# Performance work log

Measured on AMD Instinct MI355X. Metric: run time of the kernel, lower is better.

Reference implementation:

```python
import jax, jax.numpy as jnp
import numpy as np

D_MODEL = 1024
EXPANDED = 1024  # d_model * expansion_factor(1.0)
K = 3
EPS = 1e-8


def rms_norm(x, w, eps=EPS):
    return x * jax.lax.rsqrt(jnp.mean(x * x, axis=-1, keepdims=True) + eps) * w


def setup_inputs() -> dict:
    key = jax.random.key(0)
    ks = jax.random.split(key, 8)
    b, t = 4, 4096
    u = jax.random.normal(ks[0], (b, t, D_MODEL), dtype=jnp.float32)
    s_in = 1.0 / np.sqrt(D_MODEL)
    s_out = 1.0 / np.sqrt(EXPANDED)
    W_in = jax.random.uniform(ks[1], (2 * EXPANDED, D_MODEL), jnp.float32, -s_in, s_in)
    b_in = jax.random.uniform(ks[2], (2 * EXPANDED,), jnp.float32, -s_in, s_in)
    in_norm_w = jnp.ones((2 * EXPANDED,), jnp.float32)
    s_conv = 1.0 / np.sqrt(K)  # groups=expanded_dim -> fan_in = K
    conv_w = jax.random.uniform(ks[3], (EXPANDED, 1, K), jnp.float32, -s_conv, s_conv)
    conv_b = jax.random.uniform(ks[4], (EXPANDED,), jnp.float32, -s_conv, s_conv)
    W_out = jax.random.uniform(ks[5], (D_MODEL, EXPANDED), jnp.float32, -s_out, s_out)
    b_out = jax.random.uniform(ks[6], (D_MODEL,), jnp.float32, -s_out, s_out)
    out_norm_w = jnp.ones((D_MODEL,), jnp.float32)
    return {
        "u": u, "W_in": W_in, "b_in": b_in, "in_norm_w": in_norm_w,
        "conv_w": conv_w, "conv_b": conv_b,
        "W_out": W_out, "b_out": b_out, "out_norm_w": out_norm_w,
    }


def reference(u, W_in, b_in, in_norm_w, conv_w, conv_b, W_out, b_out, out_norm_w):
    # in_proj + RMSNorm
    xv = rms_norm(jnp.einsum('btd,ed->bte', u, W_in) + b_in, in_norm_w)  # [b,t,2E]
    x, v = jnp.split(xv, 2, axis=-1)  # each [b,t,E]
    # depthwise 'same' conv along time: NCH layout
    x_f = jnp.transpose(x, (0, 2, 1))  # [b,E,t]
    pad = (K - 1) // 2
    y = jax.lax.conv_general_dilated(
        x_f, conv_w, window_strides=(1,), padding=[(pad, pad)],
        dimension_numbers=('NCH', 'OIH', 'NCH'), feature_group_count=EXPANDED)
    y = y + conv_b[None, :, None]
    x_mixed = jnp.transpose(y, (0, 2, 1))  # [b,t,E]
    gated = v * x_mixed
    out = rms_norm(jnp.einsum('bte,de->btd', gated, W_out) + b_out, out_norm_w)
    return out
```

## Files before the change

### kernel.cpp

```cpp
#include <hip/hip_runtime.h>

#define BT    16384
#define TSEQ  4096
#define DM    1024
#define EXP   1024
#define N1    2048
#define KDIM  1024
#define EPSV  1e-8f

typedef __bf16 bf16x8 __attribute__((ext_vector_type(8)));
typedef float f32x16 __attribute__((ext_vector_type(16)));
typedef unsigned short u16x8 __attribute__((ext_vector_type(8)));

#define AS1CAST(p) ((__attribute__((address_space(1))) void*)(p))
#define AS3CAST(p) ((__attribute__((address_space(3))) void*)(p))

__device__ __forceinline__ unsigned short f2bf(float f) {
    unsigned int u = __float_as_uint(f);
    u += 0x7fffu + ((u >> 16) & 1u);
    return (unsigned short)(u >> 16);
}

__global__ __launch_bounds__(256) void k_f2bf(const float* __restrict__ in,
                                              unsigned short* __restrict__ out,
                                              int n4) {
    int i = blockIdx.x * 256 + threadIdx.x;
    if (i >= n4) return;
    float4 v = ((const float4*)in)[i];
    ushort4 o;
    o.x = f2bf(v.x); o.y = f2bf(v.y); o.z = f2bf(v.z); o.w = f2bf(v.w);
    ((ushort4*)out)[i] = o;
}

template <int BF16_OUT>
__device__ __forceinline__ void gemm_body(const unsigned short* __restrict__ A,
                                          const unsigned short* __restrict__ Bw,
                                          const float* __restrict__ bias,
                                          unsigned short* __restrict__ Cb,
                                          float* __restrict__ Cf,
                                          float* __restrict__ ssq,
                                          int N) {
    __shared__ unsigned short sA[128 * 32];
    __shared__ unsigned short sB[128 * 32];

    const int tid  = threadIdx.x;
    const int lane = tid & 63;
    const int wv   = tid >> 6;
    const int wm   = wv >> 1, wn = wv & 1;
    const int row0 = blockIdx.y * 128, col0 = blockIdx.x * 128;

    const int rA = tid >> 2, cA = (tid & 3) * 8;
    const unsigned short* aP = A  + (size_t)(row0 + rA) * KDIM + cA;
    const unsigned short* bP = Bw + (size_t)(col0 + rA) * KDIM + cA;
    unsigned short* lA0 = sA + (wv * 64) * 8;
    unsigned short* lA1 = sA + (256 + wv * 64) * 8;
    unsigned short* lB0 = sB + (wv * 64) * 8;
    unsigned short* lB1 = sB + (256 + wv * 64) * 8;

    const int ln = lane & 31;
    const int hi = lane >> 5;
    const int abase = (wm * 64 + ln) * 32 + hi * 8;
    const int bbase = (wn * 64 + ln) * 32 + hi * 8;

    f32x16 acc[2][2] = {};

    for (int kt = 0; kt < KDIM / 32; ++kt) {
        __syncthreads();
        const unsigned short* ap = aP + kt * 32;
        const unsigned short* bp = bP + kt * 32;
        __builtin_amdgcn_global_load_lds(AS1CAST(ap), AS3CAST(lA0), 16, 0, 0);
        __builtin_amdgcn_global_load_lds(AS1CAST(ap + (size_t)64 * KDIM), AS3CAST(lA1), 16, 0, 0);
        __builtin_amdgcn_global_load_lds(AS1CAST(bp), AS3CAST(lB0), 16, 0, 0);
        __builtin_amdgcn_global_load_lds(AS1CAST(bp + (size_t)64 * KDIM), AS3CAST(lB1), 16, 0, 0);
        __syncthreads();

        bf16x8 aF[2][2], bF[2][2];
#pragma unroll
        for (int i = 0; i < 2; ++i)
#pragma unroll
            for (int ks = 0; ks < 2; ++ks) {
                aF[i][ks] = *(const bf16x8*)&sA[abase + i * 32 * 32 + ks * 16];
                bF[i][ks] = *(const bf16x8*)&sB[bbase + i * 32 * 32 + ks * 16];
            }
#pragma unroll
        for (int ks = 0; ks < 2; ++ks)
#pragma unroll
            for (int i = 0; i < 2; ++i)
#pragma unroll
                for (int j = 0; j < 2; ++j)
                    acc[i][j] = __builtin_amdgcn_mfma_f32_32x32x16_bf16(
                        aF[i][ks], bF[j][ks], acc[i][j], 0, 0, 0);
    }

    const int c0 = col0 + wn * 64 + ln;
    const float bs0 = bias[c0], bs1 = bias[c0 + 32];

#pragma unroll
    for (int i = 0; i < 2; ++i) {
        const int rbase = row0 + wm * 64 + i * 32 + 4 * hi;
#pragma unroll
        for (int reg = 0; reg < 16; ++reg) {
            const int gm = rbase + (reg & 3) + 8 * (reg >> 2);
            float v0 = acc[i][0][reg] + bs0;
            float v1 = acc[i][1][reg] + bs1;
            float p = v0 * v0 + v1 * v1;
#pragma unroll
            for (int off = 1; off < 32; off <<= 1) p += __shfl_xor(p, off, 64);
            if (ln == 0) atomicAdd(&ssq[gm], p);
            size_t base = (size_t)gm * N + c0;
            if (BF16_OUT) {
                Cb[base]      = f2bf(v0);
                Cb[base + 32] = f2bf(v1);
            } else {
                Cf[base]      = v0;
                Cf[base + 32] = v1;
            }
        }
    }
}

__global__ __launch_bounds__(256) void k_gemm_in(const unsigned short* __restrict__ A,
                                                 const unsigned short* __restrict__ Bw,
                                                 const float* __restrict__ bias,
                                                 unsigned short* __restrict__ Cb,
                                                 float* __restrict__ ssq) {
    gemm_body<1>(A, Bw, bias, Cb, nullptr, ssq, N1);
}

__global__ __launch_bounds__(256) void k_gemm_out(const unsigned short* __restrict__ A,
                                                  const unsigned short* __restrict__ Bw,
                                                  const float* __restrict__ bias,
                                                  float* __restrict__ Cf,
                                                  float* __restrict__ ssq) {
    gemm_body<0>(A, Bw, bias, nullptr, Cf, ssq, DM);
}

__global__ __launch_bounds__(256) void k_conv_gate(const unsigned short* __restrict__ z,
                                                   const float* __restrict__ ssq1,
                                                   const float* __restrict__ inw,
                                                   const float* __restrict__ cw,
                                                   const float* __restrict__ cb,
                                                   unsigned short* __restrict__ g) {
    const int tok = blockIdx.x * 2 + (threadIdx.x >> 7);
    const int e8  = (threadIdx.x & 127) * 8;
    const int t   = tok & (TSEQ - 1);

    const float rs0 = rsqrtf(ssq1[tok] * (1.0f / N1) + EPSV);
    const int tm = (t > 0) ? tok - 1 : tok;
    const int tp = (t < TSEQ - 1) ? tok + 1 : tok;
    const float rsm = (t > 0) ? rsqrtf(ssq1[tm] * (1.0f / N1) + EPSV) : 0.0f;
    const float rsp = (t < TSEQ - 1) ? rsqrtf(ssq1[tp] * (1.0f / N1) + EPSV) : 0.0f;

    bf16x8 xm = *(const bf16x8*)(z + (size_t)tm * N1 + e8);
    bf16x8 x0 = *(const bf16x8*)(z + (size_t)tok * N1 + e8);
    bf16x8 xp = *(const bf16x8*)(z + (size_t)tp * N1 + e8);
    bf16x8 vv = *(const bf16x8*)(z + (size_t)tok * N1 + EXP + e8);

    u16x8 ov;
#pragma unroll
    for (int p = 0; p < 8; ++p) {
        const int e = e8 + p;
        const float we  = inw[e];
        const float wvv = inw[EXP + e];
        const float w0 = cw[e * 3], w1 = cw[e * 3 + 1], w2 = cw[e * 3 + 2];
        float y = w0 * ((float)xm[p] * rsm * we)
                + w1 * ((float)x0[p] * rs0 * we)
                + w2 * ((float)xp[p] * rsp * we)
                + cb[e];
        float vn = (float)vv[p] * rs0 * wvv;
        ov[p] = f2bf(vn * y);
    }
    *(u16x8*)(g + (size_t)tok * EXP + e8) = ov;
}

__global__ __launch_bounds__(256) void k_outnorm(float* __restrict__ o,
                                                 const float* __restrict__ ssq2,
                                                 const float* __restrict__ onw) {
    const int idx = blockIdx.x * 256 + threadIdx.x;
    const int tok = idx >> 8;
    const int d4  = (idx & 255) * 4;
    const float rs = rsqrtf(ssq2[tok] * (1.0f / DM) + EPSV);
    float4 v = ((float4*)o)[idx];
    float4 w = *(const float4*)(onw + d4);
    v.x *= rs * w.x; v.y *= rs * w.y; v.z *= rs * w.z; v.w *= rs * w.w;
    ((float4*)o)[idx] = v;
}

extern "C" void kernel_launch(void* const* d_in, const int* in_sizes, int n_in,
                              void* d_out, int out_size, void* d_ws, size_t ws_size,
                              hipStream_t stream) {
    const float* u     = (const float*)d_in[0];
    const float* W_in  = (const float*)d_in[1];
    const float* b_in  = (const float*)d_in[2];
    const float* inw   = (const float*)d_in[3];
    const float* cw    = (const float*)d_in[4];
    const float* cb    = (const float*)d_in[5];
    const float* W_out = (const float*)d_in[6];
    const float* b_out = (const float*)d_in[7];
    const float* onw   = (const float*)d_in[8];
    float* out = (float*)d_out;

    char* ws = (char*)d_ws;
    unsigned short* u_bf    = (unsigned short*)ws; ws += (size_t)BT * DM * 2;
    unsigned short* Win_bf  = (unsigned short*)ws; ws += (size_t)N1 * DM * 2;
    unsigned short* Wout_bf = (unsigned short*)ws; ws += (size_t)DM * EXP * 2;
    unsigned short* z_bf    = (unsigned short*)ws; ws += (size_t)BT * N1 * 2;
    unsigned short* g_bf    = (unsigned short*)ws; ws += (size_t)BT * EXP * 2;
    float* ssq1 = (float*)ws; ws += (size_t)BT * 4;
    float* ssq2 = (float*)ws; ws += (size_t)BT * 4;

    hipMemsetAsync(ssq1, 0, (size_t)BT * 2 * sizeof(float), stream);

    k_f2bf<<<(BT * DM / 4 + 255) / 256, 256, 0, stream>>>(u, u_bf, BT * DM / 4);
    k_f2bf<<<(N1 * DM / 4 + 255) / 256, 256, 0, stream>>>(W_in, Win_bf, N1 * DM / 4);
    k_f2bf<<<(DM * EXP / 4 + 255) / 256, 256, 0, stream>>>(W_out, Wout_bf, DM * EXP / 4);

    dim3 gA(N1 / 128, BT / 128);
    k_gemm_in<<<gA, 256, 0, stream>>>(u_bf, Win_bf, b_in, z_bf, ssq1);

    k_conv_gate<<<BT / 2, 256, 0, stream>>>(z_bf, ssq1, inw, cw, cb, g_bf);

    dim3 gC(DM / 128, BT / 128);
    k_gemm_out<<<gC, 256, 0, stream>>>(g_bf, Wout_bf, b_out, out, ssq2);

    k_outnorm<<<BT, 256, 0, stream>>>(out, ssq2, onw);

    (void)in_sizes; (void)n_in; (void)out_size; (void)ws_size;
}
```

Before: 350.4 us.

## Double GEMM K-tile to 64 with XOR-swizzled LDS layout and merge conversion launches

The GEMM K-step grows from 32 to 64, which halves the number of barrier pairs per tile. The LDS layout gets a row-dependent XOR-style swizzle of the 16-byte chunks so that the MFMA fragment reads avoid bank conflicts. The three fp32-to-bf16 conversion kernels are also merged into one launch. LDS use doubles to 32KB per block, which may lower occupancy, and there is still no double buffering.

```diff
diff --git a/kernel.cpp b/kernel.cpp
--- a/kernel.cpp
+++ b/kernel.cpp
@@ -21,11 +21,15 @@
     return (unsigned short)(u >> 16);
 }
 
-__global__ __launch_bounds__(256) void k_f2bf(const float* __restrict__ in,
-                                              unsigned short* __restrict__ out,
-                                              int n4) {
+__global__ __launch_bounds__(256) void k_f2bf3(const float* __restrict__ i0, unsigned short* __restrict__ o0, int n0,
+                                               const float* __restrict__ i1, unsigned short* __restrict__ o1, int n1,
+                                               const float* __restrict__ i2, unsigned short* __restrict__ o2, int n2) {
     int i = blockIdx.x * 256 + threadIdx.x;
-    if (i >= n4) return;
+    const float* in; unsigned short* out;
+    if (i < n0)                { in = i0; out = o0; }
+    else if (i < n0 + n1)      { in = i1; out = o1; i -= n0; }
+    else if (i < n0 + n1 + n2) { in = i2; out = o2; i -= n0 + n1; }
+    else return;
     float4 v = ((const float4*)in)[i];
     ushort4 o;
     o.x = f2bf(v.x); o.y = f2bf(v.y); o.z = f2bf(v.z); o.w = f2bf(v.w);
@@ -40,8 +44,8 @@
                                           float* __restrict__ Cf,
                                           float* __restrict__ ssq,
                                           int N) {
-    __shared__ unsigned short sA[128 * 32];
-    __shared__ unsigned short sB[128 * 32];
+    __shared__ unsigned short sA[128 * 64];
+    __shared__ unsigned short sB[128 * 64];
 
     const int tid  = threadIdx.x;
     const int lane = tid & 63;
@@ -49,47 +53,56 @@
     const int wm   = wv >> 1, wn = wv & 1;
     const int row0 = blockIdx.y * 128, col0 = blockIdx.x * 128;
 
-    const int rA = tid >> 2, cA = (tid & 3) * 8;
-    const unsigned short* aP = A  + (size_t)(row0 + rA) * KDIM + cA;
-    const unsigned short* bP = Bw + (size_t)(col0 + rA) * KDIM + cA;
-    unsigned short* lA0 = sA + (wv * 64) * 8;
-    unsigned short* lA1 = sA + (256 + wv * 64) * 8;
-    unsigned short* lB0 = sB + (wv * 64) * 8;
-    unsigned short* lB1 = sB + (256 + wv * 64) * 8;
+    const int p7 = tid & 7;
+    const unsigned short* aPtr[4];
+    const unsigned short* bPtr[4];
+#pragma unroll
+    for (int b = 0; b < 4; ++b) {
+        const int r = (b * 256 + tid) >> 3;
+        const int q = (p7 - r) & 7;
+        aPtr[b] = A  + (size_t)(row0 + r) * KDIM + q * 8;
+        bPtr[b] = Bw + (size_t)(col0 + r) * KDIM + q * 8;
+    }
+    unsigned short* lA[4];
+    unsigned short* lB[4];
+#pragma unroll
+    for (int b = 0; b < 4; ++b) {
+        lA[b] = sA + (b * 256 + wv * 64) * 8;
+        lB[b] = sB + (b * 256 + wv * 64) * 8;
+    }
 
     const int ln = lane & 31;
     const int hi = lane >> 5;
-    const int abase = (wm * 64 + ln) * 32 + hi * 8;
-    const int bbase = (wn * 64 + ln) * 32 + hi * 8;
+    const int arow0 = (wm * 64 + ln) * 64;
+    const int brow0 = (wn * 64 + ln) * 64;
 
     f32x16 acc[2][2] = {};
 
-    for (int kt = 0; kt < KDIM / 32; ++kt) {
+    for (int kt = 0; kt < KDIM / 64; ++kt) {
         __syncthreads();
-        const unsigned short* ap = aP + kt * 32;
-        const unsigned short* bp = bP + kt * 32;
-        __builtin_amdgcn_global_load_lds(AS1CAST(ap), AS3CAST(lA0), 16, 0, 0);
-        __builtin_amdgcn_global_load_lds(AS1CAST(ap + (size_t)64 * KDIM), AS3CAST(lA1), 16, 0, 0);
-        __builtin_amdgcn_global_load_lds(AS1CAST(bp), AS3CAST(lB0), 16, 0, 0);
-        __builtin_amdgcn_global_load_lds(AS1CAST(bp + (size_t)64 * KDIM), AS3CAST(lB1), 16, 0, 0);
+#pragma unroll
+        for (int b = 0; b < 4; ++b) {
+            __builtin_amdgcn_global_load_lds(AS1CAST(aPtr[b] + kt * 64), AS3CAST(lA[b]), 16, 0, 0);
+            __builtin_amdgcn_global_load_lds(AS1CAST(bPtr[b] + kt * 64), AS3CAST(lB[b]), 16, 0, 0);
+        }
         __syncthreads();
 
-        bf16x8 aF[2][2], bF[2][2];
-#pragma unroll
-        for (int i = 0; i < 2; ++i)
-#pragma unroll
-            for (int ks = 0; ks < 2; ++ks) {
-                aF[i][ks] = *(const bf16x8*)&sA[abase + i * 32 * 32 + ks * 16];
-                bF[i][ks] = *(const bf16x8*)&sB[bbase + i * 32 * 32 + ks * 16];
+#pragma unroll
+        for (int ks = 0; ks < 4; ++ks) {
+            const int sw = (((ks * 2 + hi) + ln) & 7) * 8;
+            bf16x8 aF[2], bF[2];
+#pragma unroll
+            for (int i = 0; i < 2; ++i) {
+                aF[i] = *(const bf16x8*)&sA[arow0 + i * 32 * 64 + sw];
+                bF[i] = *(const bf16x8*)&sB[brow0 + i * 32 * 64 + sw];
             }
-#pragma unroll
-        for (int ks = 0; ks < 2; ++ks)
 #pragma unroll
             for (int i = 0; i < 2; ++i)
 #pragma unroll
                 for (int j = 0; j < 2; ++j)
                     acc[i][j] = __builtin_amdgcn_mfma_f32_32x32x16_bf16(
-                        aF[i][ks], bF[j][ks], acc[i][j], 0, 0, 0);
+                        aF[i], bF[j], acc[i][j], 0, 0, 0);
+        }
     }
 
     const int c0 = col0 + wn * 64 + ln;
@@ -211,9 +224,10 @@
 
     hipMemsetAsync(ssq1, 0, (size_t)BT * 2 * sizeof(float), stream);
 
-    k_f2bf<<<(BT * DM / 4 + 255) / 256, 256, 0, stream>>>(u, u_bf, BT * DM / 4);
-    k_f2bf<<<(N1 * DM / 4 + 255) / 256, 256, 0, stream>>>(W_in, Win_bf, N1 * DM / 4);
-    k_f2bf<<<(DM * EXP / 4 + 255) / 256, 256, 0, stream>>>(W_out, Wout_bf, DM * EXP / 4);
+    const int n0 = BT * DM / 4, n1c = N1 * DM / 4, n2c = DM * EXP / 4;
+    k_f2bf3<<<(n0 + n1c + n2c + 255) / 256, 256, 0, stream>>>(u, u_bf, n0,
+                                                              W_in, Win_bf, n1c,
+                                                              W_out, Wout_bf, n2c);
 
     dim3 gA(N1 / 128, BT / 128);
     k_gemm_in<<<gA, 256, 0, stream>>>(u_bf, Win_bf, b_in, z_bf, ssq1);
```

Result: faster. 324.2 us (-7.5%).
